# Performance work log

Measured on AMD Instinct MI355X. Metric: run time of the kernel, lower is better.

Reference implementation:

```python
import jax, jax.numpy as jnp
import numpy as np

B, N, C, H = 2, 2048, 768, 12
D = C // H  # head dim = 64


def _rotate_half(x):
    d2 = x.shape[-1] // 2
    x1, x2 = x[..., :d2], x[..., d2:]
    return jnp.concatenate([-x2, x1], axis=-1)


def _apply_rope(x, sin, cos):
    # x: [B,H,N,D], sin/cos: [N,D] -> broadcast over (B,H)
    return x * cos[None, None] + _rotate_half(x) * sin[None, None]


def setup_inputs() -> dict:
    key = jax.random.key(0)
    ks = jax.random.split(key, 7)
    x = jax.random.normal(ks[0], (B, N, C), dtype=jnp.float32)
    sin_spatial = jax.random.normal(ks[1], (N, D), dtype=jnp.float32)
    cos_spatial = jax.random.normal(ks[2], (N, D), dtype=jnp.float32)
    s = 1.0 / np.sqrt(C)
    W_qkv = jax.random.uniform(ks[3], (C, 3 * C), jnp.float32, -s, s)
    b_qkv = jax.random.uniform(ks[4], (3 * C,), jnp.float32, -s, s)
    W_out = jax.random.uniform(ks[5], (C, C), jnp.float32, -s, s)
    b_out = jax.random.uniform(ks[6], (C,), jnp.float32, -s, s)
    return {"x": x, "sin_spatial": sin_spatial, "cos_spatial": cos_spatial,
            "W_qkv": W_qkv, "b_qkv": b_qkv, "W_out": W_out, "b_out": b_out}


def reference(x, sin_spatial, cos_spatial, W_qkv, b_qkv, W_out, b_out):
    qkv = x @ W_qkv + b_qkv                       # [B,N,3C]
    qkv = qkv.reshape(B, N, 3, H, D).transpose(2, 0, 3, 1, 4)  # [3,B,H,N,D]
    q, k, v = qkv[0], qkv[1], qkv[2]
    q = _apply_rope(q, sin_spatial, cos_spatial)
    k = _apply_rope(k, sin_spatial, cos_spatial)
    att = jnp.einsum('bhqd,bhkd->bhqk', q, k) * (D ** -0.5)
    att = jax.nn.softmax(att, axis=-1)            # dropout is identity (eval)
    y = jnp.einsum('bhqk,bhkd->bhqd', att, v)     # [B,H,N,D]
    y = y.transpose(0, 2, 1, 3).reshape(B, N, C)
    return y @ W_out + b_out
```

## Files before the change

kernel.cpp:

```cpp
#include <hip/hip_runtime.h>
#include <hip/hip_bf16.h>

#define BB 2
#define NN 2048
#define CC 768
#define HH 12
#define DD 64
#define MM 4096
#define N3 2304

typedef __attribute__((ext_vector_type(8))) short bf16x8;
typedef __attribute__((ext_vector_type(4))) float f32x4;

#define QSCALE 0.18033688011112043f

__device__ __forceinline__ unsigned short f2bf(float f) {
    union { float f; unsigned u; } v; v.f = f;
    unsigned r = v.u + 0x7FFFu + ((v.u >> 16) & 1u);
    return (unsigned short)(r >> 16);
}

__device__ __forceinline__ float exp2_hw(float x) {
    float r;
    asm("v_exp_f32 %0, %1" : "=v"(r) : "v"(x));
    return r;
}

__device__ __forceinline__ bf16x8 ld_frag(const unsigned short* p) {
    bf16x8 r;
    __builtin_memcpy(&r, p, 8);
    __builtin_memcpy((char*)&r + 8, p + 16, 8);
    return r;
}

__global__ void k_cvt(const float* __restrict__ s, unsigned short* __restrict__ d, int n4) {
    int i = blockIdx.x * blockDim.x + threadIdx.x;
    int st = gridDim.x * blockDim.x;
    for (; i < n4; i += st) {
        float4 v = ((const float4*)s)[i];
        ushort4 o;
        o.x = f2bf(v.x); o.y = f2bf(v.y); o.z = f2bf(v.z); o.w = f2bf(v.w);
        ((ushort4*)d)[i] = o;
    }
}

__global__ void k_cvtT(const float* __restrict__ s, unsigned short* __restrict__ d,
                       int R, int Cc) {
    __shared__ unsigned short t[64][72];
    const int c0 = blockIdx.x * 64, r0 = blockIdx.y * 64;
    const int tr = threadIdx.x >> 4;
    const int tc = (threadIdx.x & 15) * 4;
#pragma unroll
    for (int i = 0; i < 4; i++) {
        int r = tr + i * 16;
        float4 v = *(const float4*)(s + (size_t)(r0 + r) * Cc + c0 + tc);
        t[tc + 0][r] = f2bf(v.x);
        t[tc + 1][r] = f2bf(v.y);
        t[tc + 2][r] = f2bf(v.z);
        t[tc + 3][r] = f2bf(v.w);
    }
    __syncthreads();
    const int wr = threadIdx.x >> 2;
    const int wc = (threadIdx.x & 3) * 16;
    *(uint4*)(d + (size_t)(c0 + wr) * R + r0 + wc)     = *(uint4*)&t[wr][wc];
    *(uint4*)(d + (size_t)(c0 + wr) * R + r0 + wc + 8) = *(uint4*)&t[wr][wc + 8];
}

__launch_bounds__(256)
__global__ void k_qkv(const unsigned short* __restrict__ xb,
                      const unsigned short* __restrict__ wt,
                      const float* __restrict__ bias,
                      const float* __restrict__ sinp,
                      const float* __restrict__ cosp,
                      unsigned short* __restrict__ qws,
                      unsigned short* __restrict__ kws,
                      unsigned short* __restrict__ vws) {
    __shared__ unsigned short As[128][40];
    __shared__ unsigned short Bs[64][40];
    const int tid = threadIdx.x;
    const int lane = tid & 63, w = tid >> 6;
    const int ql = lane & 15, lg = lane >> 4;
    const int row0 = blockIdx.x * 128;
    const int j0 = blockIdx.y * 64;

    f32x4 acc[2][4];
#pragma unroll
    for (int a = 0; a < 2; a++)
#pragma unroll
        for (int b = 0; b < 4; b++) acc[a][b] = f32x4{0.f, 0.f, 0.f, 0.f};

    const int ar = tid >> 1, ac = (tid & 1) * 16;
    const int jr = tid >> 2, kc = (tid & 3) * 8;

    for (int k0 = 0; k0 < CC; k0 += 32) {
        uint4 av0 = *(const uint4*)(xb + (size_t)(row0 + ar) * CC + k0 + ac);
        uint4 av1 = *(const uint4*)(xb + (size_t)(row0 + ar) * CC + k0 + ac + 8);
        uint4 bv  = *(const uint4*)(wt + (size_t)(j0 + jr) * CC + k0 + kc);
        *(uint4*)&As[ar][ac]     = av0;
        *(uint4*)&As[ar][ac + 8] = av1;
        *(uint4*)&Bs[jr][kc]     = bv;
        __syncthreads();

        bf16x8 af[2], bfr[4];
#pragma unroll
        for (int fr = 0; fr < 2; fr++) af[fr] = ld_frag(&As[w * 32 + fr * 16 + ql][lg * 4]);
#pragma unroll
        for (int fn = 0; fn < 4; fn++) bfr[fn] = ld_frag(&Bs[fn * 16 + ql][lg * 4]);
#pragma unroll
        for (int fr = 0; fr < 2; fr++)
#pragma unroll
            for (int fn = 0; fn < 4; fn++)
                acc[fr][fn] = __builtin_amdgcn_mfma_f32_16x16x32_bf16(af[fr], bfr[fn], acc[fr][fn], 0, 0, 0);
        __syncthreads();
    }

    float vals[2][4][4];
#pragma unroll
    for (int fr = 0; fr < 2; fr++)
#pragma unroll
        for (int fn = 0; fn < 4; fn++) {
            float bj = bias[j0 + fn * 16 + ql];
#pragma unroll
            for (int r = 0; r < 4; r++) vals[fr][fn][r] = acc[fr][fn][r] + bj;
        }
    const int t = j0 / CC;
    const int h = (j0 % CC) >> 6;
    if (t < 2) {
        unsigned short* outp = (t == 0) ? qws : kws;
        const float qs = (t == 0) ? QSCALE : 1.0f;
#pragma unroll
        for (int fr = 0; fr < 2; fr++)
#pragma unroll
            for (int r = 0; r < 4; r++) {
                int m = row0 + w * 32 + fr * 16 + lg * 4 + r;
                int b = m >> 11, n = m & (NN - 1);
#pragma unroll
                for (int fn = 0; fn < 4; fn++) {
                    int d = fn * 16 + ql;
                    float cv = cosp[n * DD + d], sv = sinp[n * DD + d];
                    float other = vals[fr][fn ^ 2][r];
                    float rv = (vals[fr][fn][r] * cv + ((fn < 2) ? -other : other) * sv) * qs;
                    outp[((size_t)(b * HH + h) * NN + n) * DD + d] = f2bf(rv);
                }
            }
    } else {
#pragma unroll
        for (int fr = 0; fr < 2; fr++)
#pragma unroll
            for (int r = 0; r < 4; r++) {
                int m = row0 + w * 32 + fr * 16 + lg * 4 + r;
                int b = m >> 11, n = m & (NN - 1);
#pragma unroll
                for (int fn = 0; fn < 4; fn++) {
                    int d = fn * 16 + ql;
                    vws[((size_t)(b * HH + h) * DD + d) * NN + n] = f2bf(vals[fr][fn][r]);
                }
            }
    }
}

__launch_bounds__(256)
__global__ void k_attn(const unsigned short* __restrict__ qws,
                       const unsigned short* __restrict__ kws,
                       const unsigned short* __restrict__ vws,
                       unsigned short* __restrict__ yws) {
    __shared__ unsigned short Ks[64][72];
    __shared__ unsigned short Vs[64][72];
    const int tid = threadIdx.x;
    const int lane = tid & 63, w = tid >> 6;
    const int ql = lane & 15, lg = lane >> 4;
    const int bh = blockIdx.y;
    const int qw = blockIdx.x * 64 + w * 16;
    const unsigned short* Qp = qws + (size_t)bh * NN * DD;
    const unsigned short* Kp = kws + (size_t)bh * NN * DD;
    const unsigned short* Vp = vws + (size_t)bh * DD * NN;

    bf16x8 qf[2];
#pragma unroll
    for (int kb = 0; kb < 2; kb++)
        qf[kb] = ld_frag(Qp + (size_t)(qw + ql) * DD + kb * 32 + lg * 4);

    f32x4 oacc[4];
#pragma unroll
    for (int a = 0; a < 4; a++) oacc[a] = f32x4{0.f, 0.f, 0.f, 0.f};
    float mrun = -1e30f, lrun = 0.f;

    const int sr = tid >> 2, sc = (tid & 3) * 16;

    for (int kt = 0; kt < NN / 64; kt++) {
        *(uint4*)&Ks[sr][sc]     = *(const uint4*)(Kp + (size_t)(kt * 64 + sr) * DD + sc);
        *(uint4*)&Ks[sr][sc + 8] = *(const uint4*)(Kp + (size_t)(kt * 64 + sr) * DD + sc + 8);
        *(uint4*)&Vs[sr][sc]     = *(const uint4*)(Vp + (size_t)sr * NN + kt * 64 + sc);
        *(uint4*)&Vs[sr][sc + 8] = *(const uint4*)(Vp + (size_t)sr * NN + kt * 64 + sc + 8);
        __syncthreads();

        f32x4 sacc[4];
#pragma unroll
        for (int a = 0; a < 4; a++) sacc[a] = f32x4{0.f, 0.f, 0.f, 0.f};
        __builtin_amdgcn_s_setprio(1);
#pragma unroll
        for (int kb = 0; kb < 2; kb++) {
            bf16x8 kf[4];
#pragma unroll
            for (int fr = 0; fr < 4; fr++) kf[fr] = ld_frag(&Ks[fr * 16 + ql][kb * 32 + lg * 4]);
#pragma unroll
            for (int fr = 0; fr < 4; fr++)
                sacc[fr] = __builtin_amdgcn_mfma_f32_16x16x32_bf16(kf[fr], qf[kb], sacc[fr], 0, 0, 0);
        }
        __builtin_amdgcn_s_setprio(0);

        float m0 = fmaxf(fmaxf(sacc[0][0], sacc[0][1]), fmaxf(sacc[0][2], sacc[0][3]));
        float m1 = fmaxf(fmaxf(sacc[1][0], sacc[1][1]), fmaxf(sacc[1][2], sacc[1][3]));
        float m2 = fmaxf(fmaxf(sacc[2][0], sacc[2][1]), fmaxf(sacc[2][2], sacc[2][3]));
        float m3 = fmaxf(fmaxf(sacc[3][0], sacc[3][1]), fmaxf(sacc[3][2], sacc[3][3]));
        float tm = fmaxf(fmaxf(m0, m1), fmaxf(m2, m3));
        tm = fmaxf(tm, __shfl_xor(tm, 16));
        tm = fmaxf(tm, __shfl_xor(tm, 32));
        if (__any(tm > mrun + 8.0f)) {
            float mn = fmaxf(mrun, tm);
            float scl = exp2_hw(mrun - mn);
            lrun *= scl;
#pragma unroll
            for (int db = 0; db < 4; db++) oacc[db] *= scl;
            mrun = mn;
        }
        float ts = 0.f;
#pragma unroll
        for (int fr = 0; fr < 4; fr++)
#pragma unroll
            for (int r = 0; r < 4; r++) {
                float p = exp2_hw(sacc[fr][r] - mrun);
                sacc[fr][r] = p;
                ts += p;
            }
        ts += __shfl_xor(ts, 16);
        ts += __shfl_xor(ts, 32);
        lrun += ts;

        bf16x8 pB[2];
#pragma unroll
        for (int kkb = 0; kkb < 2; kkb++) {
            bf16x8 t8;
#pragma unroll
            for (int e = 0; e < 8; e++)
                t8[e] = (short)f2bf(sacc[kkb * 2 + (e >> 2)][e & 3]);
            pB[kkb] = t8;
        }

        __builtin_amdgcn_s_setprio(1);
#pragma unroll
        for (int db = 0; db < 4; db++) {
            bf16x8 va[2];
#pragma unroll
            for (int kkb = 0; kkb < 2; kkb++) va[kkb] = ld_frag(&Vs[db * 16 + ql][kkb * 32 + lg * 4]);
#pragma unroll
            for (int kkb = 0; kkb < 2; kkb++)
                oacc[db] = __builtin_amdgcn_mfma_f32_16x16x32_bf16(va[kkb], pB[kkb], oacc[db], 0, 0, 0);
        }
        __builtin_amdgcn_s_setprio(0);
        __syncthreads();
    }

    const int b = bh / HH, h = bh % HH;
    float inv = 1.0f / lrun;
    int q = qw + ql;
#pragma unroll
    for (int db = 0; db < 4; db++)
#pragma unroll
        for (int r = 0; r < 4; r++) {
            int d = db * 16 + lg * 4 + r;
            yws[(size_t)(b * NN + q) * CC + h * DD + d] = f2bf(oacc[db][r] * inv);
        }
}

__launch_bounds__(256)
__global__ void k_out(const unsigned short* __restrict__ yb,
                      const unsigned short* __restrict__ wt,
                      const float* __restrict__ bias,
                      float* __restrict__ out) {
    __shared__ unsigned short As[128][40];
    __shared__ unsigned short Bs[64][40];
    const int tid = threadIdx.x;
    const int lane = tid & 63, w = tid >> 6;
    const int ql = lane & 15, lg = lane >> 4;
    const int row0 = blockIdx.x * 128;
    const int j0 = blockIdx.y * 64;

    f32x4 acc[2][4];
#pragma unroll
    for (int a = 0; a < 2; a++)
#pragma unroll
        for (int b = 0; b < 4; b++) acc[a][b] = f32x4{0.f, 0.f, 0.f, 0.f};

    const int ar = tid >> 1, ac = (tid & 1) * 16;
    const int jr = tid >> 2, kc = (tid & 3) * 8;

    for (int k0 = 0; k0 < CC; k0 += 32) {
        uint4 av0 = *(const uint4*)(yb + (size_t)(row0 + ar) * CC + k0 + ac);
        uint4 av1 = *(const uint4*)(yb + (size_t)(row0 + ar) * CC + k0 + ac + 8);
        uint4 bv  = *(const uint4*)(wt + (size_t)(j0 + jr) * CC + k0 + kc);
        *(uint4*)&As[ar][ac]     = av0;
        *(uint4*)&As[ar][ac + 8] = av1;
        *(uint4*)&Bs[jr][kc]     = bv;
        __syncthreads();

        bf16x8 af[2], bfr[4];
#pragma unroll
        for (int fr = 0; fr < 2; fr++) af[fr] = ld_frag(&As[w * 32 + fr * 16 + ql][lg * 4]);
#pragma unroll
        for (int fn = 0; fn < 4; fn++) bfr[fn] = ld_frag(&Bs[fn * 16 + ql][lg * 4]);
#pragma unroll
        for (int fr = 0; fr < 2; fr++)
#pragma unroll
            for (int fn = 0; fn < 4; fn++)
                acc[fr][fn] = __builtin_amdgcn_mfma_f32_16x16x32_bf16(af[fr], bfr[fn], acc[fr][fn], 0, 0, 0);
        __syncthreads();
    }

#pragma unroll
    for (int fr = 0; fr < 2; fr++)
#pragma unroll
        for (int fn = 0; fn < 4; fn++) {
            float bj = bias[j0 + fn * 16 + ql];
#pragma unroll
            for (int r = 0; r < 4; r++) {
                int m = row0 + w * 32 + fr * 16 + lg * 4 + r;
                out[(size_t)m * CC + j0 + fn * 16 + ql] = acc[fr][fn][r] + bj;
            }
        }
}

extern "C" void kernel_launch(void* const* d_in, const int* in_sizes, int n_in,
                              void* d_out, int out_size, void* d_ws, size_t ws_size,
                              hipStream_t stream) {
    const float* x    = (const float*)d_in[0];
    const float* sinp = (const float*)d_in[1];
    const float* cosp = (const float*)d_in[2];
    const float* wqkv = (const float*)d_in[3];
    const float* bqkv = (const float*)d_in[4];
    const float* wout = (const float*)d_in[5];
    const float* bout = (const float*)d_in[6];
    float* out = (float*)d_out;
    char* ws = (char*)d_ws;

    unsigned short* xb  = (unsigned short*)(ws);
    unsigned short* wqb = (unsigned short*)(ws + 6291456);
    unsigned short* wob = (unsigned short*)(ws + 9830400);
    unsigned short* qws = (unsigned short*)(ws + 11010048);
    unsigned short* kws = (unsigned short*)(ws + 17301504);
    unsigned short* vws = (unsigned short*)(ws + 23592960);
    unsigned short* yws = (unsigned short*)(ws + 29884416);
    if (ws_size < 36175872) return;

    k_cvt<<<dim3(512), dim3(256), 0, stream>>>(x, xb, MM * CC / 4);
    k_cvtT<<<dim3(36, 12), dim3(256), 0, stream>>>(wqkv, wqb, CC, N3);
    k_cvtT<<<dim3(12, 12), dim3(256), 0, stream>>>(wout, wob, CC, CC);
    k_qkv<<<dim3(32, 36), dim3(256), 0, stream>>>(xb, wqb, bqkv, sinp, cosp, qws, kws, vws);
    k_attn<<<dim3(32, 24), dim3(256), 0, stream>>>(qws, kws, vws, yws);
    k_out<<<dim3(32, 12), dim3(256), 0, stream>>>(yws, wob, bout, out);
}
```

Baseline: 142.4 us.

## Enlarge GEMM tiles, double-buffer swizzled attention K/V, vectorize output stores

The QKV and output GEMMs now use 128x128 block tiles with a 2x2 warp layout, so each warp computes a 64x64 sub-tile and fewer blocks launch. The attention kernel double-buffers K/V tiles in XOR-swizzled shared memory and prefetches the next tile into registers while computing the current one, which drops one barrier per iteration and avoids bank conflicts. It also switches the P conversion to the library bf16 round-to-nearest and stores the attention output as 4-wide vectors. In exchange, the GEMMs give a much smaller grid on a large-CU device with more registers per thread, and attention uses more LDS.

```diff
diff --git a/kernel.cpp b/kernel.cpp
--- a/kernel.cpp
+++ b/kernel.cpp
@@ -20,6 +20,12 @@
     return (unsigned short)(r >> 16);
 }
 
+__device__ __forceinline__ unsigned short f2bf_rn(float f) {
+    union { __hip_bfloat16 h; unsigned short u; } v;
+    v.h = __float2bfloat16(f);
+    return v.u;
+}
+
 __device__ __forceinline__ float exp2_hw(float x) {
     float r;
     asm("v_exp_f32 %0, %1" : "=v"(r) : "v"(x));
@@ -30,6 +36,17 @@
     bf16x8 r;
     __builtin_memcpy(&r, p, 8);
     __builtin_memcpy((char*)&r + 8, p + 16, 8);
+    return r;
+}
+
+__device__ __forceinline__ bf16x8 ld_frag_sw(const unsigned short* base, int row, int colsh) {
+    const int rx = row & 7;
+    const unsigned short* p0 = base + row * 64 + ((((colsh) >> 3) ^ rx) << 3) + (colsh & 7);
+    const int c2 = colsh + 16;
+    const unsigned short* p1 = base + row * 64 + (((c2 >> 3) ^ rx) << 3) + (c2 & 7);
+    bf16x8 r;
+    __builtin_memcpy(&r, p0, 8);
+    __builtin_memcpy((char*)&r + 8, p1, 8);
     return r;
 }
 
@@ -76,63 +93,66 @@
                       unsigned short* __restrict__ kws,
                       unsigned short* __restrict__ vws) {
     __shared__ unsigned short As[128][40];
-    __shared__ unsigned short Bs[64][40];
+    __shared__ unsigned short Bs[128][40];
     const int tid = threadIdx.x;
     const int lane = tid & 63, w = tid >> 6;
     const int ql = lane & 15, lg = lane >> 4;
+    const int wr = w >> 1, wc = w & 1;
     const int row0 = blockIdx.x * 128;
-    const int j0 = blockIdx.y * 64;
-
-    f32x4 acc[2][4];
-#pragma unroll
-    for (int a = 0; a < 2; a++)
+    const int j0 = blockIdx.y * 128;
+
+    f32x4 acc[4][4];
+#pragma unroll
+    for (int a = 0; a < 4; a++)
 #pragma unroll
         for (int b = 0; b < 4; b++) acc[a][b] = f32x4{0.f, 0.f, 0.f, 0.f};
 
     const int ar = tid >> 1, ac = (tid & 1) * 16;
-    const int jr = tid >> 2, kc = (tid & 3) * 8;
 
     for (int k0 = 0; k0 < CC; k0 += 32) {
-        uint4 av0 = *(const uint4*)(xb + (size_t)(row0 + ar) * CC + k0 + ac);
-        uint4 av1 = *(const uint4*)(xb + (size_t)(row0 + ar) * CC + k0 + ac + 8);
-        uint4 bv  = *(const uint4*)(wt + (size_t)(j0 + jr) * CC + k0 + kc);
-        *(uint4*)&As[ar][ac]     = av0;
-        *(uint4*)&As[ar][ac + 8] = av1;
-        *(uint4*)&Bs[jr][kc]     = bv;
+        uint4 a0 = *(const uint4*)(xb + (size_t)(row0 + ar) * CC + k0 + ac);
+        uint4 a1 = *(const uint4*)(xb + (size_t)(row0 + ar) * CC + k0 + ac + 8);
+        uint4 b0 = *(const uint4*)(wt + (size_t)(j0 + ar) * CC + k0 + ac);
+        uint4 b1 = *(const uint4*)(wt + (size_t)(j0 + ar) * CC + k0 + ac + 8);
+        *(uint4*)&As[ar][ac]     = a0;
+        *(uint4*)&As[ar][ac + 8] = a1;
+        *(uint4*)&Bs[ar][ac]     = b0;
+        *(uint4*)&Bs[ar][ac + 8] = b1;
         __syncthreads();
 
-        bf16x8 af[2], bfr[4];
-#pragma unroll
-        for (int fr = 0; fr < 2; fr++) af[fr] = ld_frag(&As[w * 32 + fr * 16 + ql][lg * 4]);
-#pragma unroll
-        for (int fn = 0; fn < 4; fn++) bfr[fn] = ld_frag(&Bs[fn * 16 + ql][lg * 4]);
-#pragma unroll
-        for (int fr = 0; fr < 2; fr++)
+        bf16x8 af[4], bfr[4];
+#pragma unroll
+        for (int fr = 0; fr < 4; fr++) af[fr] = ld_frag(&As[wr * 64 + fr * 16 + ql][lg * 4]);
+#pragma unroll
+        for (int fn = 0; fn < 4; fn++) bfr[fn] = ld_frag(&Bs[wc * 64 + fn * 16 + ql][lg * 4]);
+#pragma unroll
+        for (int fr = 0; fr < 4; fr++)
 #pragma unroll
             for (int fn = 0; fn < 4; fn++)
                 acc[fr][fn] = __builtin_amdgcn_mfma_f32_16x16x32_bf16(af[fr], bfr[fn], acc[fr][fn], 0, 0, 0);
         __syncthreads();
     }
 
-    float vals[2][4][4];
-#pragma unroll
-    for (int fr = 0; fr < 2; fr++)
+    const int j0w = j0 + wc * 64;
+    const int t = j0w / CC;
+    const int h = (j0w % CC) >> 6;
+    float vals[4][4][4];
+#pragma unroll
+    for (int fr = 0; fr < 4; fr++)
 #pragma unroll
         for (int fn = 0; fn < 4; fn++) {
-            float bj = bias[j0 + fn * 16 + ql];
+            float bj = bias[j0w + fn * 16 + ql];
 #pragma unroll
             for (int r = 0; r < 4; r++) vals[fr][fn][r] = acc[fr][fn][r] + bj;
         }
-    const int t = j0 / CC;
-    const int h = (j0 % CC) >> 6;
     if (t < 2) {
         unsigned short* outp = (t == 0) ? qws : kws;
         const float qs = (t == 0) ? QSCALE : 1.0f;
 #pragma unroll
-        for (int fr = 0; fr < 2; fr++)
+        for (int fr = 0; fr < 4; fr++)
 #pragma unroll
             for (int r = 0; r < 4; r++) {
-                int m = row0 + w * 32 + fr * 16 + lg * 4 + r;
+                int m = row0 + wr * 64 + fr * 16 + lg * 4 + r;
                 int b = m >> 11, n = m & (NN - 1);
 #pragma unroll
                 for (int fn = 0; fn < 4; fn++) {
@@ -145,10 +165,10 @@
             }
     } else {
 #pragma unroll
-        for (int fr = 0; fr < 2; fr++)
+        for (int fr = 0; fr < 4; fr++)
 #pragma unroll
             for (int r = 0; r < 4; r++) {
-                int m = row0 + w * 32 + fr * 16 + lg * 4 + r;
+                int m = row0 + wr * 64 + fr * 16 + lg * 4 + r;
                 int b = m >> 11, n = m & (NN - 1);
 #pragma unroll
                 for (int fn = 0; fn < 4; fn++) {
@@ -164,8 +184,8 @@
                        const unsigned short* __restrict__ kws,
                        const unsigned short* __restrict__ vws,
                        unsigned short* __restrict__ yws) {
-    __shared__ unsigned short Ks[64][72];
-    __shared__ unsigned short Vs[64][72];
+    __shared__ unsigned short Ks[2][64 * 64];
+    __shared__ unsigned short Vs[2][64 * 64];
     const int tid = threadIdx.x;
     const int lane = tid & 63, w = tid >> 6;
     const int ql = lane & 15, lg = lane >> 4;
@@ -185,14 +205,33 @@
     for (int a = 0; a < 4; a++) oacc[a] = f32x4{0.f, 0.f, 0.f, 0.f};
     float mrun = -1e30f, lrun = 0.f;
 
-    const int sr = tid >> 2, sc = (tid & 3) * 16;
-
-    for (int kt = 0; kt < NN / 64; kt++) {
-        *(uint4*)&Ks[sr][sc]     = *(const uint4*)(Kp + (size_t)(kt * 64 + sr) * DD + sc);
-        *(uint4*)&Ks[sr][sc + 8] = *(const uint4*)(Kp + (size_t)(kt * 64 + sr) * DD + sc + 8);
-        *(uint4*)&Vs[sr][sc]     = *(const uint4*)(Vp + (size_t)sr * NN + kt * 64 + sc);
-        *(uint4*)&Vs[sr][sc + 8] = *(const uint4*)(Vp + (size_t)sr * NN + kt * 64 + sc + 8);
-        __syncthreads();
+    const int srow = tid >> 3;
+    const int sunit = tid & 7;
+
+#pragma unroll
+    for (int p = 0; p < 2; p++) {
+        int row = p * 32 + srow;
+        int off = row * 64 + (((sunit) ^ (row & 7)) << 3);
+        *(uint4*)&Ks[0][off] = *(const uint4*)(Kp + (size_t)row * DD + sunit * 8);
+        *(uint4*)&Vs[0][off] = *(const uint4*)(Vp + (size_t)row * NN + sunit * 8);
+    }
+    __syncthreads();
+
+    const int NT = NN / 64;
+    int cur = 0;
+    for (int kt = 0; kt < NT; kt++) {
+        uint4 kn[2], vn[2];
+        const bool hasn = (kt + 1 < NT);
+        if (hasn) {
+#pragma unroll
+            for (int p = 0; p < 2; p++) {
+                int row = p * 32 + srow;
+                kn[p] = *(const uint4*)(Kp + (size_t)((kt + 1) * 64 + row) * DD + sunit * 8);
+                vn[p] = *(const uint4*)(Vp + (size_t)row * NN + (kt + 1) * 64 + sunit * 8);
+            }
+        }
+        const unsigned short* Kc = Ks[cur];
+        const unsigned short* Vc = Vs[cur];
 
         f32x4 sacc[4];
 #pragma unroll
@@ -202,7 +241,7 @@
         for (int kb = 0; kb < 2; kb++) {
             bf16x8 kf[4];
 #pragma unroll
-            for (int fr = 0; fr < 4; fr++) kf[fr] = ld_frag(&Ks[fr * 16 + ql][kb * 32 + lg * 4]);
+            for (int fr = 0; fr < 4; fr++) kf[fr] = ld_frag_sw(Kc, fr * 16 + ql, kb * 32 + lg * 4);
 #pragma unroll
             for (int fr = 0; fr < 4; fr++)
                 sacc[fr] = __builtin_amdgcn_mfma_f32_16x16x32_bf16(kf[fr], qf[kb], sacc[fr], 0, 0, 0);
@@ -243,7 +282,7 @@
             bf16x8 t8;
 #pragma unroll
             for (int e = 0; e < 8; e++)
-                t8[e] = (short)f2bf(sacc[kkb * 2 + (e >> 2)][e & 3]);
+                t8[e] = (short)f2bf_rn(sacc[kkb * 2 + (e >> 2)][e & 3]);
             pB[kkb] = t8;
         }
 
@@ -252,25 +291,39 @@
         for (int db = 0; db < 4; db++) {
             bf16x8 va[2];
 #pragma unroll
-            for (int kkb = 0; kkb < 2; kkb++) va[kkb] = ld_frag(&Vs[db * 16 + ql][kkb * 32 + lg * 4]);
+            for (int kkb = 0; kkb < 2; kkb++) va[kkb] = ld_frag_sw(Vc, db * 16 + ql, kkb * 32 + lg * 4);
 #pragma unroll
             for (int kkb = 0; kkb < 2; kkb++)
                 oacc[db] = __builtin_amdgcn_mfma_f32_16x16x32_bf16(va[kkb], pB[kkb], oacc[db], 0, 0, 0);
         }
         __builtin_amdgcn_s_setprio(0);
-        __syncthreads();
+
+        if (hasn) {
+#pragma unroll
+            for (int p = 0; p < 2; p++) {
+                int row = p * 32 + srow;
+                int off = row * 64 + (((sunit) ^ (row & 7)) << 3);
+                *(uint4*)&Ks[cur ^ 1][off] = kn[p];
+                *(uint4*)&Vs[cur ^ 1][off] = vn[p];
+            }
+            __syncthreads();
+            cur ^= 1;
+        }
     }
 
     const int b = bh / HH, h = bh % HH;
     float inv = 1.0f / lrun;
     int q = qw + ql;
-#pragma unroll
-    for (int db = 0; db < 4; db++)
-#pragma unroll
-        for (int r = 0; r < 4; r++) {
-            int d = db * 16 + lg * 4 + r;
-            yws[(size_t)(b * NN + q) * CC + h * DD + d] = f2bf(oacc[db][r] * inv);
-        }
+    unsigned short* yp = yws + (size_t)(b * NN + q) * CC + h * DD + lg * 4;
+#pragma unroll
+    for (int db = 0; db < 4; db++) {
+        ushort4 o;
+        o.x = f2bf(oacc[db][0] * inv);
+        o.y = f2bf(oacc[db][1] * inv);
+        o.z = f2bf(oacc[db][2] * inv);
+        o.w = f2bf(oacc[db][3] * inv);
+        *(ushort4*)(yp + db * 16) = o;
+    }
 }
 
 __launch_bounds__(256)
@@ -279,38 +332,40 @@
                       const float* __restrict__ bias,
                       float* __restrict__ out) {
     __shared__ unsigned short As[128][40];
-    __shared__ unsigned short Bs[64][40];
+    __shared__ unsigned short Bs[128][40];
     const int tid = threadIdx.x;
     const int lane = tid & 63, w = tid >> 6;
     const int ql = lane & 15, lg = lane >> 4;
+    const int wr = w >> 1, wc = w & 1;
     const int row0 = blockIdx.x * 128;
-    const int j0 = blockIdx.y * 64;
-
-    f32x4 acc[2][4];
-#pragma unroll
-    for (int a = 0; a < 2; a++)
+    const int j0 = blockIdx.y * 128;
+
+    f32x4 acc[4][4];
+#pragma unroll
+    for (int a = 0; a < 4; a++)
 #pragma unroll
         for (int b = 0; b < 4; b++) acc[a][b] = f32x4{0.f, 0.f, 0.f, 0.f};
 
     const int ar = tid >> 1, ac = (tid & 1) * 16;
-    const int jr = tid >> 2, kc = (tid & 3) * 8;
 
     for (int k0 = 0; k0 < CC; k0 += 32) {
-        uint4 av0 = *(const uint4*)(yb + (size_t)(row0 + ar) * CC + k0 + ac);
-        uint4 av1 = *(const uint4*)(yb + (size_t)(row0 + ar) * CC + k0 + ac + 8);
-        uint4 bv  = *(const uint4*)(wt + (size_t)(j0 + jr) * CC + k0 + kc);
-        *(uint4*)&As[ar][ac]     = av0;
-        *(uint4*)&As[ar][ac + 8] = av1;
-        *(uint4*)&Bs[jr][kc]     = bv;
+        uint4 a0 = *(const uint4*)(yb + (size_t)(row0 + ar) * CC + k0 + ac);
+        uint4 a1 = *(const uint4*)(yb + (size_t)(row0 + ar) * CC + k0 + ac + 8);
+        uint4 b0 = *(const uint4*)(wt + (size_t)(j0 + ar) * CC + k0 + ac);
+        uint4 b1 = *(const uint4*)(wt + (size_t)(j0 + ar) * CC + k0 + ac + 8);
+        *(uint4*)&As[ar][ac]     = a0;
+        *(uint4*)&As[ar][ac + 8] = a1;
+        *(uint4*)&Bs[ar][ac]     = b0;
+        *(uint4*)&Bs[ar][ac + 8] = b1;
         __syncthreads();
 
-        bf16x8 af[2], bfr[4];
-#pragma unroll
-        for (int fr = 0; fr < 2; fr++) af[fr] = ld_frag(&As[w * 32 + fr * 16 + ql][lg * 4]);
-#pragma unroll
-        for (int fn = 0; fn < 4; fn++) bfr[fn] = ld_frag(&Bs[fn * 16 + ql][lg * 4]);
-#pragma unroll
-        for (int fr = 0; fr < 2; fr++)
+        bf16x8 af[4], bfr[4];
+#pragma unroll
+        for (int fr = 0; fr < 4; fr++) af[fr] = ld_frag(&As[wr * 64 + fr * 16 + ql][lg * 4]);
+#pragma unroll
+        for (int fn = 0; fn < 4; fn++) bfr[fn] = ld_frag(&Bs[wc * 64 + fn * 16 + ql][lg * 4]);
+#pragma unroll
+        for (int fr = 0; fr < 4; fr++)
 #pragma unroll
             for (int fn = 0; fn < 4; fn++)
                 acc[fr][fn] = __builtin_amdgcn_mfma_f32_16x16x32_bf16(af[fr], bfr[fn], acc[fr][fn], 0, 0, 0);
@@ -318,14 +373,14 @@
     }
 
 #pragma unroll
-    for (int fr = 0; fr < 2; fr++)
+    for (int fr = 0; fr < 4; fr++)
 #pragma unroll
         for (int fn = 0; fn < 4; fn++) {
-            float bj = bias[j0 + fn * 16 + ql];
+            float bj = bias[j0 + wc * 64 + fn * 16 + ql];
 #pragma unroll
             for (int r = 0; r < 4; r++) {
-                int m = row0 + w * 32 + fr * 16 + lg * 4 + r;
-                out[(size_t)m * CC + j0 + fn * 16 + ql] = acc[fr][fn][r] + bj;
+                int m = row0 + wr * 64 + fr * 16 + lg * 4 + r;
+                out[(size_t)m * CC + j0 + wc * 64 + fn * 16 + ql] = acc[fr][fn][r] + bj;
             }
         }
 }
@@ -355,7 +410,7 @@
     k_cvt<<<dim3(512), dim3(256), 0, stream>>>(x, xb, MM * CC / 4);
     k_cvtT<<<dim3(36, 12), dim3(256), 0, stream>>>(wqkv, wqb, CC, N3);
     k_cvtT<<<dim3(12, 12), dim3(256), 0, stream>>>(wout, wob, CC, CC);
-    k_qkv<<<dim3(32, 36), dim3(256), 0, stream>>>(xb, wqb, bqkv, sinp, cosp, qws, kws, vws);
+    k_qkv<<<dim3(32, 18), dim3(256), 0, stream>>>(xb, wqb, bqkv, sinp, cosp, qws, kws, vws);
     k_attn<<<dim3(32, 24), dim3(256), 0, stream>>>(qws, kws, vws, yws);
-    k_out<<<dim3(32, 12), dim3(256), 0, stream>>>(yws, wob, bout, out);
-}
+    k_out<<<dim3(32, 6), dim3(256), 0, stream>>>(yws, wob, bout, out);
+}
```

Result: slower. 195.6 us (+37.3%).
